# Kernel tuning notes

Hardware: AMD Instinct MI355X
Metric: run time of the kernel (lower is better)

The kernel has to match this reference:

```python
import jax, jax.numpy as jnp
import numpy as np

LN_EPS = 1e-5  # torch nn.LayerNorm default


def setup_inputs() -> dict:
    key = jax.random.key(0)
    ks = jax.random.split(key, 8)
    B, S, H, A, L = 32, 2048, 1024, 256, 10
    return {
        "hidden_states": jax.random.normal(ks[0], (B, S, H), dtype=jnp.float32),
        "language_ids": jax.random.randint(ks[1], (B,), 0, L, dtype=jnp.int64),
        "W1": jax.random.normal(ks[2], (L, H, A), dtype=jnp.float32) * (1.0 / np.sqrt(H)),
        "b1": jnp.zeros((L, A), dtype=jnp.float32),
        "W2": jax.random.normal(ks[3], (L, A, H), dtype=jnp.float32) * (1.0 / np.sqrt(A)),
        "b2": jnp.zeros((L, H), dtype=jnp.float32),
        "gamma": jnp.ones((L, H), dtype=jnp.float32),
        "beta": jnp.zeros((L, H), dtype=jnp.float32),
    }


def reference(hidden_states, language_ids, W1, b1, W2, b2, gamma, beta):
    # Gather each sample's language-specific adapter params: [B, ...]
    w1 = W1[language_ids]                       # [B, H, A]
    w2 = W2[language_ids]                       # [B, A, H]
    # Bottleneck MLP (dropout is identity at inference)
    h = jnp.einsum('bsh,bha->bsa', hidden_states, w1) + b1[language_ids][:, None, :]
    h = jax.nn.relu(h)
    adapted = jnp.einsum('bsa,bah->bsh', h, w2) + b2[language_ids][:, None, :]
    # Residual + per-language LayerNorm over last dim
    x = hidden_states + adapted
    mean = jnp.mean(x, axis=-1, keepdims=True)
    var = jnp.mean(jnp.square(x - mean), axis=-1, keepdims=True)
    normed = (x - mean) * jax.lax.rsqrt(var + LN_EPS)
    return normed * gamma[language_ids][:, None, :] + beta[language_ids][:, None, :]
```

## Files before the change

kernel.cpp:

```cpp
#include <hip/hip_runtime.h>

#define B_  32
#define S_  2048
#define H_  1024
#define A_  256
#define L_  10

typedef unsigned short u16;
typedef __bf16 bf16_t;
typedef bf16_t bfv8 __attribute__((ext_vector_type(8)));
typedef float  f32x4 __attribute__((ext_vector_type(4)));
typedef u16    u16x4 __attribute__((ext_vector_type(4)));

__device__ __forceinline__ u16 f2bf(float f) {
    unsigned int u = __builtin_bit_cast(unsigned int, f);
    u += 0x7FFFu + ((u >> 16) & 1u);
    return (u16)(u >> 16);
}
__device__ __forceinline__ float bf2f(u16 h) {
    unsigned int u = ((unsigned int)h) << 16;
    return __builtin_bit_cast(float, u);
}

typedef __attribute__((address_space(1))) const unsigned int gu32_t;
typedef __attribute__((address_space(3))) unsigned int lu32_t;
__device__ __forceinline__ void glds16(const void* g, void* l) {
    __builtin_amdgcn_global_load_lds((gu32_t*)g, (lu32_t*)l, 16, 0, 0);
}

__device__ __forceinline__ void split4(float4 v, u16x4& h4, u16x4& l4) {
    float a0 = v.x, a1 = v.y, a2 = v.z, a3 = v.w;
    u16 h;
    h = f2bf(a0); h4[0] = h; l4[0] = f2bf(a0 - bf2f(h));
    h = f2bf(a1); h4[1] = h; l4[1] = f2bf(a1 - bf2f(h));
    h = f2bf(a2); h4[2] = h; l4[2] = f2bf(a2 - bf2f(h));
    h = f2bf(a3); h4[3] = h; l4[3] = f2bf(a3 - bf2f(h));
}

__global__ __launch_bounds__(256) void pack_weights(
    const float* __restrict__ W1, const float* __restrict__ W2,
    u16* __restrict__ w1h, u16* __restrict__ w1l,
    u16* __restrict__ w2h, u16* __restrict__ w2l)
{
    __shared__ float lds[32][264];
    const int p = blockIdx.x;
    const float* src; int sstride; u16 *dh, *dl; size_t dbase;
    if (p < 320) {
        int lid = p >> 5, ktg = p & 31;
        src = W1 + ((size_t)lid * H_ + ktg * 32) * A_;
        sstride = A_;
        dh = w1h; dl = w1l;
        dbase = (size_t)(lid * 32 + ktg) * 8192;
    } else {
        int p2 = p - 320;
        int lid = p2 >> 5, kt = (p2 >> 2) & 7, nq = p2 & 3;
        src = W2 + ((size_t)lid * A_ + kt * 32) * H_ + nq * 256;
        sstride = H_;
        dh = w2h; dl = w2l;
        dbase = ((size_t)(lid * 8 + kt) * 64 + nq * 16) * 512;
    }
    const int t = threadIdx.x;
    #pragma unroll
    for (int j = 0; j < 8; ++j) {
        int row = j * 4 + (t >> 6);
        int c4  = (t & 63) * 4;
        float4 v = *(const float4*)(src + (size_t)row * sstride + c4);
        *(float4*)&lds[row][c4] = v;
    }
    __syncthreads();
    #pragma unroll
    for (int j = 0; j < 32; ++j) {
        int q    = j * 256 + t;
        int slot = q & 511, tl = q >> 9;
        int ln   = slot >> 3, i = slot & 7;
        int kl   = ((ln >> 4) << 3) + i;
        int n    = tl * 16 + (ln & 15);
        float v  = lds[kl][n];
        u16 hi   = f2bf(v);
        dh[dbase + q] = hi;
        dl[dbase + q] = f2bf(v - bf2f(hi));
    }
}

__global__ __launch_bounds__(512) void fused_adapter(
    const float* __restrict__ X, const int* __restrict__ langs,
    const float* __restrict__ b1, const float* __restrict__ b2,
    const float* __restrict__ gamma, const float* __restrict__ beta,
    const u16* __restrict__ w1h, const u16* __restrict__ w1l,
    const u16* __restrict__ w2h, const u16* __restrict__ w2l,
    float* __restrict__ out)
{
    extern __shared__ char smem[];
    u16*   hh    = (u16*)smem;
    u16*   hl    = (u16*)(smem + 32768);
    u16*   xbuf  = (u16*)(smem + 65536);
    u16*   w1b   = (u16*)(smem + 83968);
    u16*   w2b   = (u16*)(smem + 65536);
    float* part  = (float*)(smem + 149504);
    float* mrstd = (float*)(smem + 151552);

    const int fid = blockIdx.x;
    const int uu  = fid >> 3;
    const int b   = (fid & 7) * 4 + (uu >> 5);
    const int s0  = (uu & 31) * 64;
    const int lid = langs[b];

    const int t = threadIdx.x, lane = t & 63, wid = t >> 6;
    const int wm = wid >> 2, wn = wid & 3;
    const int lr = lane & 15, lg = lane >> 4;

    const float* Xb = X + ((size_t)(b * S_ + s0)) * H_;

    f32x4 acc1[2][4];
    #pragma unroll
    for (int mf = 0; mf < 2; ++mf)
        #pragma unroll
        for (int nf = 0; nf < 4; ++nf) acc1[mf][nf] = f32x4{0.f, 0.f, 0.f, 0.f};

    const int srow = t >> 3, skg = (t & 7) * 4;

    {
        float4 xv = *(const float4*)(Xb + (size_t)srow * H_ + skg);
        #pragma unroll
        for (int j = 0; j < 4; ++j) {
            int idx = wid * 4 + j, pl = idx >> 4, nt = idx & 15;
            const u16* g = (pl ? w1l : w1h) + ((size_t)(lid * 32 + 0) * 16 + nt) * 512 + lane * 8;
            glds16(g, w1b + ((0 * 2 + pl) * 16 + nt) * 512);
        }
        u16x4 h4, l4; split4(xv, h4, l4);
        *(u16x4*)(xbuf + srow * 72 + skg)        = h4;
        *(u16x4*)(xbuf + 4608 + srow * 72 + skg) = l4;
        __syncthreads();
    }

    #pragma unroll 1
    for (int kt = 0; kt < 32; ++kt) {
        float4 xv;
        if (kt < 31) {
            xv = *(const float4*)(Xb + (size_t)srow * H_ + (kt + 1) * 32 + skg);
            #pragma unroll
            for (int j = 0; j < 4; ++j) {
                int idx = wid * 4 + j, pl = idx >> 4, nt = idx & 15;
                const u16* g = (pl ? w1l : w1h) + ((size_t)(lid * 32 + kt + 1) * 16 + nt) * 512 + lane * 8;
                glds16(g, w1b + ((((kt + 1) & 1) * 2 + pl) * 16 + nt) * 512);
            }
        }
        bfv8 ah[2], al[2];
        #pragma unroll
        for (int mf = 0; mf < 2; ++mf) {
            int row = wm * 32 + mf * 16 + lr;
            ah[mf] = *(const bfv8*)(xbuf + row * 72 + lg * 8);
            al[mf] = *(const bfv8*)(xbuf + 4608 + row * 72 + lg * 8);
        }
        const u16* wb = w1b + (kt & 1) * 16384;
        #pragma unroll
        for (int nf = 0; nf < 4; ++nf) {
            int nt = wn * 4 + nf;
            bfv8 bh = *(const bfv8*)(wb + nt * 512 + lane * 8);
            bfv8 bl = *(const bfv8*)(wb + 8192 + nt * 512 + lane * 8);
            #pragma unroll
            for (int mf = 0; mf < 2; ++mf) {
                acc1[mf][nf] = __builtin_amdgcn_mfma_f32_16x16x32_bf16(ah[mf], bh, acc1[mf][nf], 0, 0, 0);
                acc1[mf][nf] = __builtin_amdgcn_mfma_f32_16x16x32_bf16(ah[mf], bl, acc1[mf][nf], 0, 0, 0);
                acc1[mf][nf] = __builtin_amdgcn_mfma_f32_16x16x32_bf16(al[mf], bh, acc1[mf][nf], 0, 0, 0);
            }
        }
        __syncthreads();
        if (kt < 31) {
            u16x4 h4, l4; split4(xv, h4, l4);
            *(u16x4*)(xbuf + srow * 72 + skg)        = h4;
            *(u16x4*)(xbuf + 4608 + srow * 72 + skg) = l4;
        }
        __syncthreads();
    }

    #pragma unroll
    for (int mf = 0; mf < 2; ++mf)
        #pragma unroll
        for (int nf = 0; nf < 4; ++nf) {
            int k = wn * 64 + nf * 16 + lr;
            float bias = b1[lid * A_ + k];
            #pragma unroll
            for (int r = 0; r < 4; ++r) {
                int row = wm * 32 + mf * 16 + lg * 4 + r;
                float v = acc1[mf][nf][r] + bias;
                v = v > 0.f ? v : 0.f;
                int sw = (row & 7) << 3;
                u16 hi = f2bf(v);
                hh[row * 256 + (k ^ sw)] = hi;
                hl[row * 256 + (k ^ sw)] = f2bf(v - bf2f(hi));
            }
        }
    #pragma unroll
    for (int j = 0; j < 4; ++j) {
        int idx = wid * 4 + j, pl = idx >> 4, tl = idx & 15;
        const u16* g = (pl ? w2l : w2h) + ((size_t)(lid * 8 + 0) * 64 + tl) * 512 + lane * 8;
        glds16(g, w2b + ((0 * 2 + pl) * 16 + tl) * 512);
    }
    __syncthreads();

    f32x4 acc2[2][4][4];
    #pragma unroll
    for (int mf = 0; mf < 2; ++mf)
        #pragma unroll
        for (int q = 0; q < 4; ++q)
            #pragma unroll
            for (int nf = 0; nf < 4; ++nf) acc2[mf][q][nf] = f32x4{0.f, 0.f, 0.f, 0.f};

    bfv8 a2h[2], a2l[2];
    #pragma unroll
    for (int kt = 0; kt < 8; ++kt) {
        #pragma unroll
        for (int q = 0; q < 4; ++q) {
            const int ph = kt * 4 + q, pbuf = ph & 1;
            if (ph < 31) {
                int kn = (ph + 1) >> 2, qn = (ph + 1) & 3;
                #pragma unroll
                for (int j = 0; j < 4; ++j) {
                    int idx = wid * 4 + j, pl = idx >> 4, tl = idx & 15;
                    const u16* g = (pl ? w2l : w2h) + ((size_t)(lid * 8 + kn) * 64 + qn * 16 + tl) * 512 + lane * 8;
                    glds16(g, w2b + (((pbuf ^ 1) * 2 + pl) * 16 + tl) * 512);
                }
            }
            if (q == 0) {
                #pragma unroll
                for (int mf = 0; mf < 2; ++mf) {
                    int row = wm * 32 + mf * 16 + lr;
                    int sw  = (row & 7) << 3;
                    a2h[mf] = *(const bfv8*)(hh + row * 256 + ((kt * 32 + lg * 8) ^ sw));
                    a2l[mf] = *(const bfv8*)(hl + row * 256 + ((kt * 32 + lg * 8) ^ sw));
                }
            }
            const u16* wb2 = w2b + pbuf * 16384;
            #pragma unroll
            for (int nf = 0; nf < 4; ++nf) {
                int tl = wn * 4 + nf;
                bfv8 bh = *(const bfv8*)(wb2 + tl * 512 + lane * 8);
                bfv8 bl = *(const bfv8*)(wb2 + 8192 + tl * 512 + lane * 8);
                #pragma unroll
                for (int mf = 0; mf < 2; ++mf) {
                    acc2[mf][q][nf] = __builtin_amdgcn_mfma_f32_16x16x32_bf16(a2h[mf], bh, acc2[mf][q][nf], 0, 0, 0);
                    acc2[mf][q][nf] = __builtin_amdgcn_mfma_f32_16x16x32_bf16(a2h[mf], bl, acc2[mf][q][nf], 0, 0, 0);
                    acc2[mf][q][nf] = __builtin_amdgcn_mfma_f32_16x16x32_bf16(a2l[mf], bh, acc2[mf][q][nf], 0, 0, 0);
                }
            }
            __syncthreads();
        }
    }

    float s1v[2][4], s2v[2][4];
    #pragma unroll
    for (int mf = 0; mf < 2; ++mf)
        #pragma unroll
        for (int r = 0; r < 4; ++r) { s1v[mf][r] = 0.f; s2v[mf][r] = 0.f; }

    #pragma unroll
    for (int mf = 0; mf < 2; ++mf)
        #pragma unroll
        for (int q = 0; q < 4; ++q)
            #pragma unroll
            for (int nf = 0; nf < 4; ++nf) {
                int col = (q * 16 + wn * 4 + nf) * 16 + lr;
                float bb = b2[lid * H_ + col];
                #pragma unroll
                for (int r = 0; r < 4; ++r) {
                    int row = wm * 32 + mf * 16 + lg * 4 + r;
                    float x = acc2[mf][q][nf][r] + bb + Xb[(size_t)row * H_ + col];
                    acc2[mf][q][nf][r] = x;
                    s1v[mf][r] += x; s2v[mf][r] += x * x;
                }
            }

    #pragma unroll
    for (int mf = 0; mf < 2; ++mf)
        #pragma unroll
        for (int r = 0; r < 4; ++r) {
            float a = s1v[mf][r], c = s2v[mf][r];
            #pragma unroll
            for (int m = 1; m < 16; m <<= 1) { a += __shfl_xor(a, m); c += __shfl_xor(c, m); }
            if (lr == 0) {
                int row = wm * 32 + mf * 16 + lg * 4 + r;
                part[(row * 4 + wn) * 2 + 0] = a;
                part[(row * 4 + wn) * 2 + 1] = c;
            }
        }
    __syncthreads();
    if (t < 64) {
        float a = part[(t*4+0)*2] + part[(t*4+1)*2] + part[(t*4+2)*2] + part[(t*4+3)*2];
        float c = part[(t*4+0)*2+1] + part[(t*4+1)*2+1] + part[(t*4+2)*2+1] + part[(t*4+3)*2+1];
        float mean = a * (1.f / 1024.f);
        float var  = c * (1.f / 1024.f) - mean * mean;
        mrstd[t*2]   = mean;
        mrstd[t*2+1] = rsqrtf(var + 1e-5f);
    }
    __syncthreads();

    float* ob = out + ((size_t)(b * S_ + s0)) * H_;
    #pragma unroll
    for (int q = 0; q < 4; ++q)
        #pragma unroll
        for (int nf = 0; nf < 4; ++nf) {
            int col = (q * 16 + wn * 4 + nf) * 16 + lr;
            float g  = gamma[lid * H_ + col];
            float bt = beta[lid * H_ + col];
            #pragma unroll
            for (int mf = 0; mf < 2; ++mf)
                #pragma unroll
                for (int r = 0; r < 4; ++r) {
                    int row = wm * 32 + mf * 16 + lg * 4 + r;
                    float x = acc2[mf][q][nf][r];
                    ob[(size_t)row * H_ + col] = (x - mrstd[row*2]) * mrstd[row*2+1] * g + bt;
                }
        }
}

extern "C" void kernel_launch(void* const* d_in, const int* in_sizes, int n_in,
                              void* d_out, int out_size, void* d_ws, size_t ws_size,
                              hipStream_t stream)
{
    const float* X     = (const float*)d_in[0];
    const int*   langs = (const int*)  d_in[1];
    const float* W1    = (const float*)d_in[2];
    const float* b1    = (const float*)d_in[3];
    const float* W2    = (const float*)d_in[4];
    const float* b2    = (const float*)d_in[5];
    const float* gamma = (const float*)d_in[6];
    const float* beta  = (const float*)d_in[7];
    float* out = (float*)d_out;

    char* ws = (char*)d_ws;
    u16* w1h = (u16*)(ws);
    u16* w1l = (u16*)(ws + 5242880);
    u16* w2h = (u16*)(ws + 10485760);
    u16* w2l = (u16*)(ws + 15728640);

    hipFuncSetAttribute((const void*)fused_adapter,
                        hipFuncAttributeMaxDynamicSharedMemorySize, 152064);

    hipLaunchKernelGGL(pack_weights, dim3(640), dim3(256), 0, stream,
                       W1, W2, w1h, w1l, w2h, w2l);
    hipLaunchKernelGGL(fused_adapter, dim3(1024), dim3(512), 152064, stream,
                       X, langs, b1, b2, gamma, beta, w1h, w1l, w2h, w2l, out);
}
```

Baseline: 885.7 us.

## Simplify weight packing, add occupancy hint, stop unrolling second GEMM k-loop

The weight-pack kernel now has each thread gather eight strided floats directly from global memory and write vectorized 8-wide bf16 hi/lo outputs, replacing the LDS staging pass. The fused adapter kernel gets a launch-bounds hint asking for two blocks per CU, and the outer k loop of the second GEMM is no longer unrolled, with the phase indexing rewritten to match. Both changes aim to cut register pressure and code size so occupancy can rise. The risks are register spills under the tighter bound, extra loop overhead, and uncoalesced strided reads in the pack kernel.

```diff
diff --git a/kernel.cpp b/kernel.cpp
--- a/kernel.cpp
+++ b/kernel.cpp
@@ -11,6 +11,7 @@
 typedef bf16_t bfv8 __attribute__((ext_vector_type(8)));
 typedef float  f32x4 __attribute__((ext_vector_type(4)));
 typedef u16    u16x4 __attribute__((ext_vector_type(4)));
+typedef u16    u16x8 __attribute__((ext_vector_type(8)));
 
 __device__ __forceinline__ u16 f2bf(float f) {
     unsigned int u = __builtin_bit_cast(unsigned int, f);
@@ -42,8 +43,8 @@
     u16* __restrict__ w1h, u16* __restrict__ w1l,
     u16* __restrict__ w2h, u16* __restrict__ w2l)
 {
-    __shared__ float lds[32][264];
     const int p = blockIdx.x;
+    const int t = threadIdx.x;
     const float* src; int sstride; u16 *dh, *dl; size_t dbase;
     if (p < 320) {
         int lid = p >> 5, ktg = p & 31;
@@ -59,30 +60,27 @@
         dh = w2h; dl = w2l;
         dbase = ((size_t)(lid * 8 + kt) * 64 + nq * 16) * 512;
     }
-    const int t = threadIdx.x;
-    #pragma unroll
-    for (int j = 0; j < 8; ++j) {
-        int row = j * 4 + (t >> 6);
-        int c4  = (t & 63) * 4;
-        float4 v = *(const float4*)(src + (size_t)row * sstride + c4);
-        *(float4*)&lds[row][c4] = v;
-    }
-    __syncthreads();
-    #pragma unroll
-    for (int j = 0; j < 32; ++j) {
-        int q    = j * 256 + t;
-        int slot = q & 511, tl = q >> 9;
-        int ln   = slot >> 3, i = slot & 7;
-        int kl   = ((ln >> 4) << 3) + i;
-        int n    = tl * 16 + (ln & 15);
-        float v  = lds[kl][n];
-        u16 hi   = f2bf(v);
-        dh[dbase + q] = hi;
-        dl[dbase + q] = f2bf(v - bf2f(hi));
-    }
-}
-
-__global__ __launch_bounds__(512) void fused_adapter(
+    const int ln = t & 63;
+    const int k0 = (ln >> 4) * 8;
+    const int nn = ln & 15;
+    #pragma unroll
+    for (int r = 0; r < 4; ++r) {
+        int nt = r * 4 + (t >> 6);
+        const float* s = src + (size_t)k0 * sstride + nt * 16 + nn;
+        u16x8 h8, l8;
+        #pragma unroll
+        for (int i = 0; i < 8; ++i) {
+            float v = s[(size_t)i * sstride];
+            u16 hi = f2bf(v);
+            h8[i] = hi; l8[i] = f2bf(v - bf2f(hi));
+        }
+        size_t q = dbase + (size_t)nt * 512 + (size_t)ln * 8;
+        *(u16x8*)(dh + q) = h8;
+        *(u16x8*)(dl + q) = l8;
+    }
+}
+
+__global__ __launch_bounds__(512, 2) void fused_adapter(
     const float* __restrict__ X, const int* __restrict__ langs,
     const float* __restrict__ b1, const float* __restrict__ b2,
     const float* __restrict__ gamma, const float* __restrict__ beta,
@@ -208,13 +206,13 @@
             for (int nf = 0; nf < 4; ++nf) acc2[mf][q][nf] = f32x4{0.f, 0.f, 0.f, 0.f};
 
     bfv8 a2h[2], a2l[2];
-    #pragma unroll
+    #pragma unroll 1
     for (int kt = 0; kt < 8; ++kt) {
         #pragma unroll
         for (int q = 0; q < 4; ++q) {
-            const int ph = kt * 4 + q, pbuf = ph & 1;
-            if (ph < 31) {
-                int kn = (ph + 1) >> 2, qn = (ph + 1) & 3;
+            const int pbuf = q & 1;
+            if (kt < 7 || q < 3) {
+                int kn = kt + (q == 3), qn = (q + 1) & 3;
                 #pragma unroll
                 for (int j = 0; j < 4; ++j) {
                     int idx = wid * 4 + j, pl = idx >> 4, tl = idx & 15;
```

After: 828.6 us. 6.4% less time.
